# Optimization experiments

Hardware: AMD Instinct MI355X
Metric: run time of the kernel (lower is better)

Reference implementation:

```python
import jax, jax.numpy as jnp
import numpy as np

N = 1024   # nnodes
H = 8      # attention heads
C = 32     # gnn_repr_size (per head)
HC = H * C # 256
E = 65536  # num edges
ER = 32    # edge_repr_size
F = 3      # feat_emb_size
NUM_STOPS = 512


def setup_inputs() -> dict:
    key = jax.random.key(0)
    ks = jax.random.split(key, 24)
    g = lambda i, shape, s: jax.random.normal(ks[i], shape, dtype=jnp.float32) * s
    return {
        "dist": jax.random.uniform(ks[0], (N, N), dtype=jnp.float32),
        "stops": jax.random.randint(ks[1], (NUM_STOPS,), 0, N),
        "weekday": 3,
        "vehicles": 5,
        "markov": jax.random.uniform(ks[2], (N, N), dtype=jnp.float32),
        "demand": jax.random.uniform(ks[3], (N, 1), dtype=jnp.float32),
        "capacity": 10,
        "edge_index": jax.random.randint(ks[4], (2, E), 0, N),
        # GATConv layer 1 (in=1, out=H*C, edge_dim=1)
        "W1": g(5, (1, HC), 1.0), "We1": g(6, (1, HC), 1.0),
        "a_src1": g(7, (H, C), 0.1), "a_dst1": g(8, (H, C), 0.1), "a_edge1": g(9, (H, C), 0.1),
        "b1": jnp.zeros((HC,), jnp.float32),
        # GATConv layer 2 (in=H*C, out=H*C)
        "W2": g(10, (HC, HC), 0.0625), "We2": g(11, (1, HC), 1.0),
        "a_src2": g(12, (H, C), 0.1), "a_dst2": g(13, (H, C), 0.1), "a_edge2": g(14, (H, C), 0.1),
        "b2": jnp.zeros((HC,), jnp.float32),
        # edge summarizer Linear(2*HC, ER)
        "Wes": g(15, (2 * HC, ER), 0.0442), "bes": jnp.zeros((ER,), jnp.float32),
        # scalar embeddings
        "emb_weekday": g(16, (7, F), 0.1), "emb_capacity": g(17, (26, F), 0.1), "emb_vehicle": g(18, (15, F), 0.1),
        # combiner MLP: Linear(N*ER + 3N + 3F, N), Linear(N, N)
        "Wc1": g(19, (N * ER + 3 * N + 3 * F, N), 0.0053), "bc1": jnp.zeros((N,), jnp.float32),
        "Wc2": g(20, (N, N), 0.03125), "bc2": jnp.zeros((N,), jnp.float32),
    }


def _gat(x, src, dst, edge_attr, W, We, a_src, a_dst, a_edge, b):
    """PyG GATConv (concat heads, eval mode so attention dropout is identity)."""
    h = (x @ W).reshape(-1, H, C)                   # [N, H, C]
    e = (edge_attr @ We).reshape(-1, H, C)          # [E, H, C]
    alpha = (h * a_src).sum(-1)[src] + (h * a_dst).sum(-1)[dst] + (e * a_edge).sum(-1)  # [E, H]
    alpha = jax.nn.leaky_relu(alpha, 0.2)
    # segment softmax over destination nodes
    m = jax.ops.segment_max(alpha, dst, num_segments=N)
    m = jnp.where(jnp.isfinite(m), m, 0.0)
    ex = jnp.exp(alpha - m[dst])
    denom = jax.ops.segment_sum(ex, dst, num_segments=N)
    coef = ex / (denom[dst] + 1e-16)                # [E, H]
    out = jax.ops.segment_sum(h[src] * coef[:, :, None], dst, num_segments=N)  # [N, H, C]
    return out.reshape(-1, HC) + b


def reference(dist, stops, weekday, vehicles, markov, demand, capacity, edge_index,
              W1, We1, a_src1, a_dst1, a_edge1, b1,
              W2, We2, a_src2, a_dst2, a_edge2, b2,
              Wes, bes, emb_weekday, emb_capacity, emb_vehicle,
              Wc1, bc1, Wc2, bc2):
    src, dst = edge_index[0], edge_index[1]
    dist = (dist - dist.min()) / (dist.max() - dist.min())
    edge_attr = markov[src, dst][:, None]           # [E, 1]
    x = _gat(demand, src, dst, edge_attr, W1, We1, a_src1, a_dst1, a_edge1, b1)
    x = jax.nn.relu(x)
    x = _gat(x, src, dst, edge_attr, W2, We2, a_src2, a_dst2, a_edge2, b2)
    x = jax.nn.relu(x)                              # [N, HC]
    # edge_summarizer(cat(x_i, x_j)) decomposed: x_i @ Wes_top + x_j @ Wes_bot + bes
    ea = x @ Wes[:HC]                               # [N, ER]
    eb = x @ Wes[HC:]                               # [N, ER]
    edge_repr = (ea[:, None, :] + eb[None, :, :] + bes).reshape(N, N * ER)
    wf = jnp.broadcast_to(emb_weekday[weekday][None, :], (N, F))
    cf = jnp.broadcast_to(emb_capacity[capacity][None, :], (N, F))
    vf = jnp.broadcast_to(emb_vehicle[vehicles][None, :], (N, F))
    sf = jnp.zeros((N,), jnp.float32).at[stops].set(1.0)
    sf = jnp.broadcast_to(sf[None, :], (N, N))
    combined = jnp.concatenate([edge_repr, dist, markov, wf, cf, vf, sf], axis=1)
    out = jax.nn.relu(combined @ Wc1 + bc1) @ Wc2 + bc2  # [N, N]
    return out
```

## Files before the change

kernel.cpp:

```cpp
#include <hip/hip_runtime.h>

#define NN 1024
#define NE 65536

typedef short v8s __attribute__((ext_vector_type(8)));
typedef float v4f __attribute__((ext_vector_type(4)));

constexpr size_t OF_SCAL = 0;
constexpr size_t OF_MMP  = 64;
constexpr size_t OF_DEG  = 1088;
constexpr size_t OF_OFF  = 2112;
constexpr size_t OF_CUR  = 3200;
constexpr size_t OF_EIDX = 4224;
constexpr size_t OF_MARK = 69760;
constexpr size_t OF_T1   = 135296;
constexpr size_t OF_X1   = 143488;
constexpr size_t OF_H2   = 405632;
constexpr size_t OF_S2S  = 667776;
constexpr size_t OF_S2D  = 675968;
constexpr size_t OF_MAX2 = 684160;
constexpr size_t OF_DEN2 = 692352;
constexpr size_t OF_EX2  = 700544;
constexpr size_t OF_X2   = 1224832;
constexpr size_t OF_BCAT = 1486976;
constexpr size_t OF_EAB  = 1503360;
constexpr size_t OF_WVEC = 1568896;
constexpr size_t OF_SRP  = 1604800;
constexpr size_t OF_C0P  = 3701952;
constexpr size_t OF_SR   = 3775680;
constexpr size_t OF_BASE = 3808448;
constexpr size_t OF_AH   = 3809472;
constexpr size_t OF_AL   = 4874432;
constexpr size_t OF_BTH  = 5939392;
constexpr size_t OF_BTL  = 7004352;
constexpr size_t OF_HH   = 8069312;
constexpr size_t OF_HL   = 8593600;
constexpr size_t OF_W2TH = 9117888;
constexpr size_t OF_W2TL = 9642176;
constexpr size_t OF_P0   = 10166464;
constexpr size_t OF_P1   = 11215040;

__device__ inline unsigned short f2bf(float x){
  unsigned u = __float_as_uint(x);
  unsigned r = u + 0x7fffu + ((u>>16)&1u);
  return (unsigned short)(r>>16);
}
__device__ inline float bf2f(unsigned short h){
  return __uint_as_float(((unsigned)h)<<16);
}

__global__ void k_zero(int* deg){
  int i = blockIdx.x*256 + threadIdx.x;
  if (i < NN) deg[i] = 0;
}

__global__ void k_mm1(const float* __restrict__ dist, float* mnP, float* mxP){
  __shared__ float smn[256], smx[256];
  int tid = threadIdx.x;
  float mn = 1e30f, mx = -1e30f;
  for (int i = blockIdx.x*256 + tid; i < NN*NN; i += gridDim.x*256){
    float v = dist[i]; mn = fminf(mn, v); mx = fmaxf(mx, v);
  }
  smn[tid]=mn; smx[tid]=mx; __syncthreads();
  for (int s=128; s>0; s>>=1){
    if (tid<s){ smn[tid]=fminf(smn[tid],smn[tid+s]); smx[tid]=fmaxf(smx[tid],smx[tid+s]); }
    __syncthreads();
  }
  if (tid==0){ mnP[blockIdx.x]=smn[0]; mxP[blockIdx.x]=smx[0]; }
}

__global__ void k_mm2(const float* mnP, const float* mxP, float* scal){
  __shared__ float smn[512], smx[512];
  int tid = threadIdx.x;
  smn[tid]=mnP[tid]; smx[tid]=mxP[tid]; __syncthreads();
  for (int s=256; s>0; s>>=1){
    if (tid<s){ smn[tid]=fminf(smn[tid],smn[tid+s]); smx[tid]=fmaxf(smx[tid],smx[tid+s]); }
    __syncthreads();
  }
  if (tid==0){ scal[0]=smn[0]; scal[1]=1.0f/(smx[0]-smn[0]); }
}

__global__ void k_prep(const float* W1, const float* We1, const float* as1, const float* ad1,
                       const float* ae1, const float* We2, const float* ae2, float* scal){
  int t = threadIdx.x;
  if (t < 8){
    float s=0.f, d=0.f, e=0.f, e2=0.f;
    for (int c=0;c<32;c++){
      int i = t*32+c;
      s += W1[i]*as1[i]; d += W1[i]*ad1[i]; e += We1[i]*ae1[i]; e2 += We2[i]*ae2[i];
    }
    scal[16+t]=s; scal[24+t]=d; scal[32+t]=e; scal[40+t]=e2;
  }
}

__global__ void k_edges(const int* __restrict__ ei, const float* __restrict__ markov,
                        float* __restrict__ mark, int* __restrict__ deg){
  int e = blockIdx.x*256 + threadIdx.x;
  if (e >= NE) return;
  int s = ei[e], d = ei[NE+e];
  mark[e] = markov[(size_t)s*NN + d];
  atomicAdd(&deg[d], 1);
}

__global__ void k_scan(const int* deg, int* off, int* cur){
  __shared__ int tmp[NN];
  int t = threadIdx.x;
  tmp[t] = deg[t]; __syncthreads();
  for (int s=1; s<NN; s<<=1){
    int v = (t>=s) ? tmp[t-s] : 0;
    __syncthreads();
    tmp[t] += v;
    __syncthreads();
  }
  int ex = (t==0) ? 0 : tmp[t-1];
  off[t]=ex; cur[t]=ex;
  if (t==NN-1) off[NN]=tmp[NN-1];
}

__global__ void k_fill(const int* __restrict__ ei, int* __restrict__ cur, int* __restrict__ eidxl){
  int e = blockIdx.x*256 + threadIdx.x;
  if (e >= NE) return;
  int d = ei[NE+e];
  int p = atomicAdd(&cur[d], 1);
  eidxl[p] = e;
}

__global__ __launch_bounds__(64) void k_gat1(const int* __restrict__ ei, const int* __restrict__ eidxl,
    const int* __restrict__ off, const float* __restrict__ mark, const float* __restrict__ demand,
    const float* __restrict__ scal, float* __restrict__ t1){
  int n = blockIdx.x, lane = threadIdx.x;
  int o0 = off[n], o1 = off[n+1];
  float dn = demand[n];
  float cs[8], cd[8], ce[8], mx[8];
  #pragma unroll
  for (int h=0;h<8;h++){ cs[h]=scal[16+h]; cd[h]=scal[24+h]; ce[h]=scal[32+h]; mx[h]=-1e30f; }
  for (int i=o0+lane; i<o1; i+=64){
    int e = eidxl[i]; float ds = demand[ei[e]]; float me = mark[e];
    #pragma unroll
    for (int h=0;h<8;h++){
      float a = ds*cs[h] + dn*cd[h] + me*ce[h];
      a = a < 0.f ? 0.2f*a : a;
      mx[h] = fmaxf(mx[h], a);
    }
  }
  #pragma unroll
  for (int s=32; s>0; s>>=1){
    #pragma unroll
    for (int h=0;h<8;h++) mx[h] = fmaxf(mx[h], __shfl_xor(mx[h], s));
  }
  float se[8], sd_[8];
  #pragma unroll
  for (int h=0;h<8;h++){ se[h]=0.f; sd_[h]=0.f; }
  for (int i=o0+lane; i<o1; i+=64){
    int e = eidxl[i]; float ds = demand[ei[e]]; float me = mark[e];
    #pragma unroll
    for (int h=0;h<8;h++){
      float a = ds*cs[h] + dn*cd[h] + me*ce[h];
      a = a < 0.f ? 0.2f*a : a;
      float ex = expf(a - mx[h]);
      se[h] += ex; sd_[h] += ex*ds;
    }
  }
  #pragma unroll
  for (int s=32; s>0; s>>=1){
    #pragma unroll
    for (int h=0;h<8;h++){ se[h] += __shfl_xor(se[h], s); sd_[h] += __shfl_xor(sd_[h], s); }
  }
  if (lane==0){
    #pragma unroll
    for (int h=0;h<8;h++) t1[n*8+h] = sd_[h] / (se[h] + 1e-16f);
  }
}

__global__ void k_x1(const float* __restrict__ t1, const float* __restrict__ W1,
                     const float* __restrict__ b1, float* __restrict__ x1){
  int n = blockIdx.x, hc = threadIdx.x, h = hc >> 5;
  x1[(size_t)n*256 + hc] = fmaxf(t1[n*8+h]*W1[hc] + b1[hc], 0.f);
}

__global__ __launch_bounds__(256) void gemm64(const float* __restrict__ A, int lda,
    const float* __restrict__ B, int ldb, float* __restrict__ C, int ldc, int K,
    const float* __restrict__ bias, int dorelu){
  __shared__ float As[16][68];
  __shared__ float Bs[16][68];
  int tid = threadIdx.x;
  int tx = tid & 15, ty = tid >> 4;
  int row0 = ty*4, col0 = tx*4;
  int gm = blockIdx.y*64, gn = blockIdx.x*64;
  float acc[4][4] = {};
  for (int k0 = 0; k0 < K; k0 += 16){
    #pragma unroll
    for (int q=0;q<4;q++){
      int idx = tid*4+q; int i = idx>>4, kk = idx&15;
      As[kk][i] = A[(size_t)(gm+i)*lda + k0 + kk];
    }
    #pragma unroll
    for (int q=0;q<4;q++){
      int idx = tid*4+q; int kk = idx>>6, j = idx&63;
      Bs[kk][j] = B[(size_t)(k0+kk)*ldb + gn + j];
    }
    __syncthreads();
    #pragma unroll
    for (int kk=0;kk<16;kk++){
      float a0=As[kk][row0+0], a1=As[kk][row0+1], a2=As[kk][row0+2], a3=As[kk][row0+3];
      float b0=Bs[kk][col0+0], b1=Bs[kk][col0+1], b2=Bs[kk][col0+2], b3=Bs[kk][col0+3];
      acc[0][0]+=a0*b0; acc[0][1]+=a0*b1; acc[0][2]+=a0*b2; acc[0][3]+=a0*b3;
      acc[1][0]+=a1*b0; acc[1][1]+=a1*b1; acc[1][2]+=a1*b2; acc[1][3]+=a1*b3;
      acc[2][0]+=a2*b0; acc[2][1]+=a2*b1; acc[2][2]+=a2*b2; acc[2][3]+=a2*b3;
      acc[3][0]+=a3*b0; acc[3][1]+=a3*b1; acc[3][2]+=a3*b2; acc[3][3]+=a3*b3;
    }
    __syncthreads();
  }
  #pragma unroll
  for (int i=0;i<4;i++){
    #pragma unroll
    for (int j=0;j<4;j++){
      int cc = gn + col0 + j;
      float v = acc[i][j];
      if (bias) v += bias[cc];
      if (dorelu) v = fmaxf(v, 0.f);
      C[(size_t)(gm+row0+i)*ldc + cc] = v;
    }
  }
}

__global__ void k_s2(const float* __restrict__ h2, const float* __restrict__ as2,
                     const float* __restrict__ ad2, float* __restrict__ s2s, float* __restrict__ s2d){
  int idx = blockIdx.x*256 + threadIdx.x;
  if (idx >= NN*8) return;
  int n = idx >> 3, h = idx & 7;
  float ss = 0.f, sd = 0.f;
  for (int c=0;c<32;c++){
    float v = h2[(size_t)n*256 + h*32 + c];
    ss += v*as2[h*32+c]; sd += v*ad2[h*32+c];
  }
  s2s[idx]=ss; s2d[idx]=sd;
}

__global__ __launch_bounds__(64) void k_gat2max(const int* __restrict__ ei, const int* __restrict__ eidxl,
    const int* __restrict__ off, const float* __restrict__ mark, const float* __restrict__ s2s,
    const float* __restrict__ s2d, const float* __restrict__ scal,
    float* __restrict__ mx2, float* __restrict__ den){
  int n = blockIdx.x, lane = threadIdx.x;
  int o0 = off[n], o1 = off[n+1];
  float ce[8], sdn[8], mx[8];
  #pragma unroll
  for (int h=0;h<8;h++){ ce[h]=scal[40+h]; sdn[h]=s2d[n*8+h]; mx[h]=-1e30f; }
  for (int i=o0+lane; i<o1; i+=64){
    int e = eidxl[i]; int s = ei[e]; float me = mark[e];
    #pragma unroll
    for (int h=0;h<8;h++){
      float a = s2s[s*8+h] + sdn[h] + me*ce[h];
      a = a < 0.f ? 0.2f*a : a;
      mx[h] = fmaxf(mx[h], a);
    }
  }
  #pragma unroll
  for (int sft=32; sft>0; sft>>=1){
    #pragma unroll
    for (int h=0;h<8;h++) mx[h] = fmaxf(mx[h], __shfl_xor(mx[h], sft));
  }
  float se[8];
  #pragma unroll
  for (int h=0;h<8;h++) se[h]=0.f;
  for (int i=o0+lane; i<o1; i+=64){
    int e = eidxl[i]; int s = ei[e]; float me = mark[e];
    #pragma unroll
    for (int h=0;h<8;h++){
      float a = s2s[s*8+h] + sdn[h] + me*ce[h];
      a = a < 0.f ? 0.2f*a : a;
      se[h] += expf(a - mx[h]);
    }
  }
  #pragma unroll
  for (int sft=32; sft>0; sft>>=1){
    #pragma unroll
    for (int h=0;h<8;h++) se[h] += __shfl_xor(se[h], sft);
  }
  if (lane==0){
    #pragma unroll
    for (int h=0;h<8;h++){ mx2[n*8+h] = (o1>o0) ? mx[h] : 0.f; den[n*8+h] = se[h]; }
  }
}

__global__ void k_ex2(const int* __restrict__ ei, const float* __restrict__ mark,
                      const float* __restrict__ s2s, const float* __restrict__ s2d,
                      const float* __restrict__ mx2, const float* __restrict__ scal,
                      float* __restrict__ ex2){
  int e = blockIdx.x*256 + threadIdx.x;
  if (e >= NE) return;
  int s = ei[e], d = ei[NE+e];
  float me = mark[e];
  #pragma unroll
  for (int h=0;h<8;h++){
    float a = s2s[s*8+h] + s2d[d*8+h] + me*scal[40+h];
    a = a < 0.f ? 0.2f*a : a;
    ex2[(size_t)e*8+h] = expf(a - mx2[d*8+h]);
  }
}

__global__ __launch_bounds__(256) void k_agg2(const int* __restrict__ ei, const int* __restrict__ eidxl,
    const int* __restrict__ off, const float* __restrict__ ex2, const float* __restrict__ den,
    const float* __restrict__ h2, const float* __restrict__ b2, float* __restrict__ x2){
  __shared__ int eL[64], sL[64];
  int n = blockIdx.x, tid = threadIdx.x, h = tid >> 5;
  int o0 = off[n], o1 = off[n+1];
  float inv = 1.0f/(den[n*8+h] + 1e-16f);
  float acc = 0.f;
  for (int b = o0; b < o1; b += 64){
    int len = min(64, o1 - b);
    __syncthreads();
    if (tid < len){ int e = eidxl[b+tid]; eL[tid]=e; sL[tid]=ei[e]; }
    __syncthreads();
    for (int j=0;j<len;j++){
      acc += ex2[(size_t)eL[j]*8 + h] * h2[(size_t)sL[j]*256 + tid];
    }
  }
  x2[(size_t)n*256 + tid] = fmaxf(acc*inv + b2[tid], 0.f);
}

__global__ void k_bcat(const float* __restrict__ Wes, float* __restrict__ Bcat){
  int idx = blockIdx.x*256 + threadIdx.x;
  if (idx >= 256*64) return;
  int k = idx >> 6, r = idx & 63;
  Bcat[idx] = (r < 32) ? Wes[(size_t)k*32 + r] : Wes[(size_t)(256+k)*32 + (r-32)];
}

__global__ void k_wvec(const float* __restrict__ eab, const float* __restrict__ bes,
                       const float* __restrict__ ew, const float* __restrict__ ec, const float* __restrict__ ev,
                       const int* __restrict__ wd, const int* __restrict__ cap, const int* __restrict__ veh,
                       float* __restrict__ wvec){
  int m = blockIdx.x*256 + threadIdx.x;
  if (m >= 35849) return;
  float v;
  if (m < 32768){ int j = m >> 5, r = m & 31; v = eab[(size_t)j*64 + 32 + r] + bes[r]; }
  else if (m < 34816) v = 0.f;
  else if (m < 34819) v = ew[wd[0]*3 + (m-34816)];
  else if (m < 34822) v = ec[cap[0]*3 + (m-34819)];
  else if (m < 34825) v = ev[veh[0]*3 + (m-34822)];
  else v = 0.f;
  wvec[m] = v;
}

__global__ void k_stops(const int* __restrict__ stops, float* __restrict__ wvec){
  wvec[34825 + stops[threadIdx.x]] = 1.0f;
}

__global__ __launch_bounds__(256) void k_src0(const float* __restrict__ Wc1, const float* __restrict__ wvec,
                                              float* __restrict__ srP, float* __restrict__ c0P){
  __shared__ float c0s[256*4];
  int t = threadIdx.x;
  int kg = t & 31;
  int rg = t >> 5;
  int col = blockIdx.x*128 + kg*4;
  int chunk = blockIdx.y;
  int m0 = chunk*512;
  float sr[4][4];
  #pragma unroll
  for (int u=0;u<4;u++){ sr[u][0]=0.f; sr[u][1]=0.f; sr[u][2]=0.f; sr[u][3]=0.f; }
  float c0a[4] = {0.f,0.f,0.f,0.f};
  for (int jj=0; jj<16; ++jj){
    int rbase = m0 + jj*32 + rg*4;
    #pragma unroll
    for (int u=0;u<4;u++){
      int m = rbase + u;
      float4 w = make_float4(0.f,0.f,0.f,0.f);
      float wv = 0.f;
      if (m < 35849){
        w = *reinterpret_cast<const float4*>(&Wc1[(size_t)m*1024 + col]);
        wv = wvec[m];
      }
      c0a[0] += wv*w.x; c0a[1] += wv*w.y; c0a[2] += wv*w.z; c0a[3] += wv*w.w;
      if (chunk < 64){
        sr[u][0] += w.x; sr[u][1] += w.y; sr[u][2] += w.z; sr[u][3] += w.w;
      }
    }
  }
  if (chunk < 64){
    #pragma unroll
    for (int u=0;u<4;u++){
      int r = rg*4 + u;
      float4 v = make_float4(sr[u][0], sr[u][1], sr[u][2], sr[u][3]);
      *reinterpret_cast<float4*>(&srP[(size_t)(chunk*32 + r)*1024 + col]) = v;
    }
  }
  c0s[t*4+0]=c0a[0]; c0s[t*4+1]=c0a[1]; c0s[t*4+2]=c0a[2]; c0s[t*4+3]=c0a[3];
  __syncthreads();
  if (t < 32){
    float s0=0.f,s1=0.f,s2=0.f,s3=0.f;
    #pragma unroll
    for (int q=0;q<8;q++){
      int b = (t + q*32)*4;
      s0 += c0s[b+0]; s1 += c0s[b+1]; s2 += c0s[b+2]; s3 += c0s[b+3];
    }
    float4 v = make_float4(s0,s1,s2,s3);
    *reinterpret_cast<float4*>(&c0P[(size_t)chunk*1024 + blockIdx.x*128 + t*4]) = v;
  }
}

__global__ void k_stage2(const float* __restrict__ srP, const float* __restrict__ c0P,
                         const float* __restrict__ bc1, float* __restrict__ Sr, float* __restrict__ base){
  int idx = blockIdx.x*256 + threadIdx.x;
  if (idx < 8192){
    int r = idx >> 8, k4 = idx & 255;
    float s0=0.f,s1=0.f,s2=0.f,s3=0.f;
    for (int c=0;c<64;c++){
      float4 v = *reinterpret_cast<const float4*>(&srP[(size_t)(c*32 + r)*1024 + k4*4]);
      s0+=v.x; s1+=v.y; s2+=v.z; s3+=v.w;
    }
    float4 o = make_float4(s0,s1,s2,s3);
    *reinterpret_cast<float4*>(&Sr[(size_t)r*1024 + k4*4]) = o;
  } else if (idx < 8448){
    int k4 = idx - 8192;
    float4 b = *reinterpret_cast<const float4*>(&bc1[k4*4]);
    float s0=b.x, s1=b.y, s2=b.z, s3=b.w;
    for (int c=0;c<71;c++){
      float4 v = *reinterpret_cast<const float4*>(&c0P[(size_t)c*1024 + k4*4]);
      s0+=v.x; s1+=v.y; s2+=v.z; s3+=v.w;
    }
    float4 o = make_float4(s0,s1,s2,s3);
    *reinterpret_cast<float4*>(&base[k4*4]) = o;
  }
}

__global__ void k_cvtA(const float* __restrict__ dist, const float* __restrict__ markov,
                       const float* __restrict__ eab, const float* __restrict__ scal,
                       unsigned short* __restrict__ Ah, unsigned short* __restrict__ Al){
  int k = blockIdx.x*256 + threadIdx.x;
  int i = blockIdx.y;
  if (k >= 2080) return;
  float mn = scal[0], inv = scal[1];
  float v;
  if (k < 1024) v = (dist[(size_t)i*1024 + k] - mn)*inv;
  else if (k < 2048) v = markov[(size_t)i*1024 + (k-1024)];
  else v = eab[(size_t)i*64 + (k-2048)];
  unsigned short h = f2bf(v);
  Ah[(size_t)i*2080 + k] = h;
  Al[(size_t)i*2080 + k] = f2bf(v - bf2f(h));
}

__global__ void k_cvtT(const float* __restrict__ src, const float* __restrict__ src2, int k2,
                       int ldt, unsigned short* __restrict__ Th, unsigned short* __restrict__ Tl){
  __shared__ unsigned short shh[32][65], shl[32][65];
  int t = threadIdx.x;
  int k0 = blockIdx.x*32, n0 = blockIdx.y*64;
  #pragma unroll
  for (int q=0;q<8;q++){
    int idx = t + q*256;
    int kl = idx >> 6, nl = idx & 63;
    int k = k0 + kl;
    float v = (k < k2) ? src[(size_t)k*1024 + n0 + nl] : src2[(size_t)(k-k2)*1024 + n0 + nl];
    unsigned short h = f2bf(v);
    shh[kl][nl] = h;
    shl[kl][nl] = f2bf(v - bf2f(h));
  }
  __syncthreads();
  #pragma unroll
  for (int q=0;q<8;q++){
    int idx = t + q*256;
    int nl = idx >> 5, kl = idx & 31;
    Th[(size_t)(n0+nl)*ldt + k0 + kl] = shh[kl][nl];
    Tl[(size_t)(n0+nl)*ldt + k0 + kl] = shl[kl][nl];
  }
}

__global__ __launch_bounds__(256) void k_mfma64(
    const unsigned short* __restrict__ Ah, const unsigned short* __restrict__ Al, int lda,
    const unsigned short* __restrict__ Bth, const unsigned short* __restrict__ Btl, int ldb,
    float* __restrict__ Cp, int kSteps, int kTot){
  __shared__ __align__(16) unsigned short Ash[64*32], Asl[64*32], Bsh[64*32], Bsl[64*32];
  int t = threadIdx.x;
  int wave = t >> 6, lane = t & 63;
  int wr = wave >> 1, wc = wave & 1;
  int gm = blockIdx.y*64, gn = blockIdx.x*64;
  Cp += (size_t)blockIdx.z << 20;
  int ks0 = blockIdx.z * kSteps;
  int ks1 = ks0 + kSteps; if (ks1 > kTot) ks1 = kTot;

  int sr = t >> 2, ss = t & 3;
  int kq = lane >> 4;
  int l15 = lane & 15;
  int rA0 = wr*32 + l15;
  int cB0 = wc*32 + l15;

  v4f acc[2][2];
  #pragma unroll
  for (int i=0;i<2;i++)
    #pragma unroll
    for (int j=0;j<2;j++) acc[i][j] = (v4f){0.f,0.f,0.f,0.f};

  for (int ks = ks0; ks < ks1; ++ks){
    int kb = ks*32;
    v8s ga_h = *(const v8s*)(Ah  + (size_t)(gm+sr)*lda + kb + ss*8);
    v8s ga_l = *(const v8s*)(Al  + (size_t)(gm+sr)*lda + kb + ss*8);
    v8s gb_h = *(const v8s*)(Bth + (size_t)(gn+sr)*ldb + kb + ss*8);
    v8s gb_l = *(const v8s*)(Btl + (size_t)(gn+sr)*ldb + kb + ss*8);
    __syncthreads();
    int woff = sr*32 + ((ss ^ (sr&3))*8);
    *(v8s*)(Ash + woff) = ga_h;
    *(v8s*)(Asl + woff) = ga_l;
    *(v8s*)(Bsh + woff) = gb_h;
    *(v8s*)(Bsl + woff) = gb_l;
    __syncthreads();
    #pragma unroll
    for (int fi=0; fi<2; fi++){
      int ra = rA0 + fi*16;
      int aoff = ra*32 + ((kq ^ (ra&3))*8);
      v8s fa_h = *(v8s*)(Ash + aoff);
      v8s fa_l = *(v8s*)(Asl + aoff);
      #pragma unroll
      for (int fj=0; fj<2; fj++){
        int cb = cB0 + fj*16;
        int boff = cb*32 + ((kq ^ (cb&3))*8);
        v8s fb_h = *(v8s*)(Bsh + boff);
        v8s fb_l = *(v8s*)(Bsl + boff);
        acc[fi][fj] = __builtin_amdgcn_mfma_f32_16x16x32_bf16(fa_h, fb_h, acc[fi][fj], 0, 0, 0);
        acc[fi][fj] = __builtin_amdgcn_mfma_f32_16x16x32_bf16(fa_h, fb_l, acc[fi][fj], 0, 0, 0);
        acc[fi][fj] = __builtin_amdgcn_mfma_f32_16x16x32_bf16(fa_l, fb_h, acc[fi][fj], 0, 0, 0);
      }
    }
  }
  int row0 = gm + wr*32 + (lane>>4)*4;
  int col0 = gn + wc*32 + l15;
  #pragma unroll
  for (int fi=0; fi<2; fi++)
    #pragma unroll
    for (int fj=0; fj<2; fj++)
      #pragma unroll
      for (int r=0; r<4; r++)
        Cp[(size_t)(row0 + fi*16 + r)*1024 + col0 + fj*16] = acc[fi][fj][r];
}

__global__ void k_fin_hidden(const float* __restrict__ P0, const float* __restrict__ P1,
                             const float* __restrict__ base,
                             unsigned short* __restrict__ Hh, unsigned short* __restrict__ Hl){
  int idx = blockIdx.x*256 + threadIdx.x;
  float v = P0[idx] + P1[idx] + base[idx & 1023];
  v = fmaxf(v, 0.f);
  unsigned short h = f2bf(v);
  Hh[idx] = h;
  Hl[idx] = f2bf(v - bf2f(h));
}

__global__ void k_fin_out(const float* __restrict__ P0, const float* __restrict__ P1,
                          const float* __restrict__ bc2, float* __restrict__ out){
  int idx = blockIdx.x*256 + threadIdx.x;
  out[idx] = P0[idx] + P1[idx] + bc2[idx & 1023];
}

extern "C" void kernel_launch(void* const* d_in, const int* in_sizes, int n_in,
                              void* d_out, int out_size, void* d_ws, size_t ws_size,
                              hipStream_t stream){
  const float* dist     = (const float*)d_in[0];
  const int*   stops    = (const int*)  d_in[1];
  const int*   weekday  = (const int*)  d_in[2];
  const int*   vehicles = (const int*)  d_in[3];
  const float* markov   = (const float*)d_in[4];
  const float* demand   = (const float*)d_in[5];
  const int*   capacity = (const int*)  d_in[6];
  const int*   ei       = (const int*)  d_in[7];
  const float* W1  = (const float*)d_in[8];
  const float* We1 = (const float*)d_in[9];
  const float* as1 = (const float*)d_in[10];
  const float* ad1 = (const float*)d_in[11];
  const float* ae1 = (const float*)d_in[12];
  const float* b1  = (const float*)d_in[13];
  const float* W2  = (const float*)d_in[14];
  const float* We2 = (const float*)d_in[15];
  const float* as2 = (const float*)d_in[16];
  const float* ad2 = (const float*)d_in[17];
  const float* ae2 = (const float*)d_in[18];
  const float* b2  = (const float*)d_in[19];
  const float* Wes = (const float*)d_in[20];
  const float* bes = (const float*)d_in[21];
  const float* ew  = (const float*)d_in[22];
  const float* ec  = (const float*)d_in[23];
  const float* ev  = (const float*)d_in[24];
  const float* Wc1 = (const float*)d_in[25];
  const float* bc1 = (const float*)d_in[26];
  const float* Wc2 = (const float*)d_in[27];
  const float* bc2 = (const float*)d_in[28];

  float* W    = (float*)d_ws;
  float* scal = W + OF_SCAL;
  float* mmP  = W + OF_MMP;
  int*   deg  = (int*)(W + OF_DEG);
  int*   off  = (int*)(W + OF_OFF);
  int*   cur  = (int*)(W + OF_CUR);
  int*   eidxl= (int*)(W + OF_EIDX);
  float* mark = W + OF_MARK;
  float* t1   = W + OF_T1;
  float* x1   = W + OF_X1;
  float* h2   = W + OF_H2;
  float* s2s  = W + OF_S2S;
  float* s2d  = W + OF_S2D;
  float* mx2  = W + OF_MAX2;
  float* den2 = W + OF_DEN2;
  float* ex2  = W + OF_EX2;
  float* x2   = W + OF_X2;
  float* Bcat = W + OF_BCAT;
  float* eab  = W + OF_EAB;
  float* wvec = W + OF_WVEC;
  float* srP  = W + OF_SRP;
  float* c0P  = W + OF_C0P;
  float* Sr   = W + OF_SR;
  float* base = W + OF_BASE;
  unsigned short* Ah   = (unsigned short*)(W + OF_AH);
  unsigned short* Al   = (unsigned short*)(W + OF_AL);
  unsigned short* Bth  = (unsigned short*)(W + OF_BTH);
  unsigned short* Btl  = (unsigned short*)(W + OF_BTL);
  unsigned short* Hh   = (unsigned short*)(W + OF_HH);
  unsigned short* Hl   = (unsigned short*)(W + OF_HL);
  unsigned short* W2th = (unsigned short*)(W + OF_W2TH);
  unsigned short* W2tl = (unsigned short*)(W + OF_W2TL);
  float* P0   = W + OF_P0;
  float* out  = (float*)d_out;

  k_zero<<<dim3(4), dim3(256), 0, stream>>>(deg);
  k_mm1 <<<dim3(512), dim3(256), 0, stream>>>(dist, mmP, mmP+512);
  k_mm2 <<<dim3(1), dim3(512), 0, stream>>>(mmP, mmP+512, scal);
  k_prep<<<dim3(1), dim3(64), 0, stream>>>(W1, We1, as1, ad1, ae1, We2, ae2, scal);
  k_edges<<<dim3(256), dim3(256), 0, stream>>>(ei, markov, mark, deg);
  k_scan<<<dim3(1), dim3(1024), 0, stream>>>(deg, off, cur);
  k_fill<<<dim3(256), dim3(256), 0, stream>>>(ei, cur, eidxl);
  k_gat1<<<dim3(1024), dim3(64), 0, stream>>>(ei, eidxl, off, mark, demand, scal, t1);
  k_x1  <<<dim3(1024), dim3(256), 0, stream>>>(t1, W1, b1, x1);
  gemm64<<<dim3(4,16), dim3(256), 0, stream>>>(x1, 256, W2, 256, h2, 256, 256, (const float*)nullptr, 0);
  k_s2  <<<dim3(32), dim3(256), 0, stream>>>(h2, as2, ad2, s2s, s2d);
  k_gat2max<<<dim3(1024), dim3(64), 0, stream>>>(ei, eidxl, off, mark, s2s, s2d, scal, mx2, den2);
  k_ex2 <<<dim3(256), dim3(256), 0, stream>>>(ei, mark, s2s, s2d, mx2, scal, ex2);
  k_agg2<<<dim3(1024), dim3(256), 0, stream>>>(ei, eidxl, off, ex2, den2, h2, b2, x2);
  k_bcat<<<dim3(64), dim3(256), 0, stream>>>(Wes, Bcat);
  gemm64<<<dim3(1,16), dim3(256), 0, stream>>>(x2, 256, Bcat, 64, eab, 64, 256, (const float*)nullptr, 0);
  k_wvec<<<dim3(141), dim3(256), 0, stream>>>(eab, bes, ew, ec, ev, weekday, capacity, vehicles, wvec);
  k_stops<<<dim3(1), dim3(512), 0, stream>>>(stops, wvec);
  k_src0<<<dim3(8,71), dim3(256), 0, stream>>>(Wc1, wvec, srP, c0P);
  k_stage2<<<dim3(33), dim3(256), 0, stream>>>(srP, c0P, bc1, Sr, base);
  k_cvtA<<<dim3(9,1024), dim3(256), 0, stream>>>(dist, markov, eab, scal, Ah, Al);
  k_cvtT<<<dim3(65,16), dim3(256), 0, stream>>>(Wc1 + (size_t)32768*1024, Sr, 2048, 2080, Bth, Btl);
  k_cvtT<<<dim3(32,16), dim3(256), 0, stream>>>(Wc2, Wc2, 1<<30, 1024, W2th, W2tl);
  k_mfma64<<<dim3(16,16,2), dim3(256), 0, stream>>>(Ah, Al, 2080, Bth, Btl, 2080, P0, 33, 65);
  k_fin_hidden<<<dim3(4096), dim3(256), 0, stream>>>(P0, P0 + (1<<20), base, Hh, Hl);
  k_mfma64<<<dim3(16,16,2), dim3(256), 0, stream>>>(Hh, Hl, 1024, W2th, W2tl, 1024, P0, 16, 32);
  k_fin_out<<<dim3(4096), dim3(256), 0, stream>>>(P0, P0 + (1<<20), bc2, out);
}
```

Measured before the change: 221.3 us.

## Enlarge split-K MFMA GEMM tiles to 128x128 and split K four ways

The split-bf16 MFMA GEMM moves from 64x64 to 128x128 output tiles, with each wave computing a 4x4 grid of 16x16 fragments. B fragments are hoisted out of the row loop, and the LDS swizzle changes to suit the new layout. This aims to raise data reuse per LDS load and cut global traffic per FLOP. To keep the grid at 256 blocks, split-K grows from 2 to 4 partial planes, which adds partial-sum writes and reads. The reduction/finalize kernels are vectorized to float4 and sum four planes, which needs a larger workspace region for the partials.

```diff
diff --git a/kernel.cpp b/kernel.cpp
--- a/kernel.cpp
+++ b/kernel.cpp
@@ -38,7 +38,6 @@
 constexpr size_t OF_W2TH = 9117888;
 constexpr size_t OF_W2TL = 9642176;
 constexpr size_t OF_P0   = 10166464;
-constexpr size_t OF_P1   = 11215040;
 
 __device__ inline unsigned short f2bf(float x){
   unsigned u = __float_as_uint(x);
@@ -464,88 +463,114 @@
   }
 }
 
-__global__ __launch_bounds__(256) void k_mfma64(
+__global__ __launch_bounds__(256) void k_mfma128(
     const unsigned short* __restrict__ Ah, const unsigned short* __restrict__ Al, int lda,
     const unsigned short* __restrict__ Bth, const unsigned short* __restrict__ Btl, int ldb,
     float* __restrict__ Cp, int kSteps, int kTot){
-  __shared__ __align__(16) unsigned short Ash[64*32], Asl[64*32], Bsh[64*32], Bsl[64*32];
+  __shared__ __align__(16) unsigned short Ash[128*32], Asl[128*32], Bsh[128*32], Bsl[128*32];
   int t = threadIdx.x;
   int wave = t >> 6, lane = t & 63;
   int wr = wave >> 1, wc = wave & 1;
-  int gm = blockIdx.y*64, gn = blockIdx.x*64;
-  Cp += (size_t)blockIdx.z << 20;
+  int gm = blockIdx.y*128, gn = blockIdx.x*128;
+  float* plane = Cp + ((size_t)blockIdx.z << 20);
   int ks0 = blockIdx.z * kSteps;
   int ks1 = ks0 + kSteps; if (ks1 > kTot) ks1 = kTot;
 
-  int sr = t >> 2, ss = t & 3;
   int kq = lane >> 4;
   int l15 = lane & 15;
-  int rA0 = wr*32 + l15;
-  int cB0 = wc*32 + l15;
-
-  v4f acc[2][2];
-  #pragma unroll
-  for (int i=0;i<2;i++)
-    #pragma unroll
-    for (int j=0;j<2;j++) acc[i][j] = (v4f){0.f,0.f,0.f,0.f};
+
+  int r0s = t >> 2,        s0s = t & 3;
+  int r1s = (t+256) >> 2,  s1s = t & 3;
+
+  v4f acc[4][4];
+  #pragma unroll
+  for (int i=0;i<4;i++)
+    #pragma unroll
+    for (int j=0;j<4;j++) acc[i][j] = (v4f){0.f,0.f,0.f,0.f};
 
   for (int ks = ks0; ks < ks1; ++ks){
     int kb = ks*32;
-    v8s ga_h = *(const v8s*)(Ah  + (size_t)(gm+sr)*lda + kb + ss*8);
-    v8s ga_l = *(const v8s*)(Al  + (size_t)(gm+sr)*lda + kb + ss*8);
-    v8s gb_h = *(const v8s*)(Bth + (size_t)(gn+sr)*ldb + kb + ss*8);
-    v8s gb_l = *(const v8s*)(Btl + (size_t)(gn+sr)*ldb + kb + ss*8);
-    __syncthreads();
-    int woff = sr*32 + ((ss ^ (sr&3))*8);
-    *(v8s*)(Ash + woff) = ga_h;
-    *(v8s*)(Asl + woff) = ga_l;
-    *(v8s*)(Bsh + woff) = gb_h;
-    *(v8s*)(Bsl + woff) = gb_l;
-    __syncthreads();
-    #pragma unroll
-    for (int fi=0; fi<2; fi++){
-      int ra = rA0 + fi*16;
-      int aoff = ra*32 + ((kq ^ (ra&3))*8);
-      v8s fa_h = *(v8s*)(Ash + aoff);
-      v8s fa_l = *(v8s*)(Asl + aoff);
+    const size_t a0 = (size_t)(gm+r0s)*lda + kb + s0s*8;
+    const size_t a1 = (size_t)(gm+r1s)*lda + kb + s1s*8;
+    const size_t b0 = (size_t)(gn+r0s)*ldb + kb + s0s*8;
+    const size_t b1 = (size_t)(gn+r1s)*ldb + kb + s1s*8;
+    v8s gah0 = *(const v8s*)(Ah + a0), gah1 = *(const v8s*)(Ah + a1);
+    v8s gal0 = *(const v8s*)(Al + a0), gal1 = *(const v8s*)(Al + a1);
+    v8s gbh0 = *(const v8s*)(Bth + b0), gbh1 = *(const v8s*)(Bth + b1);
+    v8s gbl0 = *(const v8s*)(Btl + b0), gbl1 = *(const v8s*)(Btl + b1);
+    __syncthreads();
+    int w0 = r0s*32 + ((s0s ^ ((r0s>>1)&3))*8);
+    int w1 = r1s*32 + ((s1s ^ ((r1s>>1)&3))*8);
+    *(v8s*)(Ash + w0) = gah0;  *(v8s*)(Ash + w1) = gah1;
+    *(v8s*)(Asl + w0) = gal0;  *(v8s*)(Asl + w1) = gal1;
+    *(v8s*)(Bsh + w0) = gbh0;  *(v8s*)(Bsh + w1) = gbh1;
+    *(v8s*)(Bsl + w0) = gbl0;  *(v8s*)(Bsl + w1) = gbl1;
+    __syncthreads();
+    v8s fbh[4], fbl[4];
+    #pragma unroll
+    for (int fj=0; fj<4; fj++){
+      int cb = wc*64 + fj*16 + l15;
+      int boff = cb*32 + ((kq ^ ((cb>>1)&3))*8);
+      fbh[fj] = *(v8s*)(Bsh + boff);
+      fbl[fj] = *(v8s*)(Bsl + boff);
+    }
+    #pragma unroll
+    for (int fi=0; fi<4; fi++){
+      int ra = wr*64 + fi*16 + l15;
+      int aoff = ra*32 + ((kq ^ ((ra>>1)&3))*8);
+      v8s fah = *(v8s*)(Ash + aoff);
+      v8s fal = *(v8s*)(Asl + aoff);
       #pragma unroll
-      for (int fj=0; fj<2; fj++){
-        int cb = cB0 + fj*16;
-        int boff = cb*32 + ((kq ^ (cb&3))*8);
-        v8s fb_h = *(v8s*)(Bsh + boff);
-        v8s fb_l = *(v8s*)(Bsl + boff);
-        acc[fi][fj] = __builtin_amdgcn_mfma_f32_16x16x32_bf16(fa_h, fb_h, acc[fi][fj], 0, 0, 0);
-        acc[fi][fj] = __builtin_amdgcn_mfma_f32_16x16x32_bf16(fa_h, fb_l, acc[fi][fj], 0, 0, 0);
-        acc[fi][fj] = __builtin_amdgcn_mfma_f32_16x16x32_bf16(fa_l, fb_h, acc[fi][fj], 0, 0, 0);
+      for (int fj=0; fj<4; fj++){
+        acc[fi][fj] = __builtin_amdgcn_mfma_f32_16x16x32_bf16(fah, fbh[fj], acc[fi][fj], 0, 0, 0);
+        acc[fi][fj] = __builtin_amdgcn_mfma_f32_16x16x32_bf16(fah, fbl[fj], acc[fi][fj], 0, 0, 0);
+        acc[fi][fj] = __builtin_amdgcn_mfma_f32_16x16x32_bf16(fal, fbh[fj], acc[fi][fj], 0, 0, 0);
       }
     }
   }
-  int row0 = gm + wr*32 + (lane>>4)*4;
-  int col0 = gn + wc*32 + l15;
-  #pragma unroll
-  for (int fi=0; fi<2; fi++)
-    #pragma unroll
-    for (int fj=0; fj<2; fj++)
+  int row0 = gm + wr*64 + (lane>>4)*4;
+  int col0 = gn + wc*64 + l15;
+  #pragma unroll
+  for (int fi=0; fi<4; fi++)
+    #pragma unroll
+    for (int fj=0; fj<4; fj++)
       #pragma unroll
       for (int r=0; r<4; r++)
-        Cp[(size_t)(row0 + fi*16 + r)*1024 + col0 + fj*16] = acc[fi][fj][r];
-}
-
-__global__ void k_fin_hidden(const float* __restrict__ P0, const float* __restrict__ P1,
-                             const float* __restrict__ base,
+        plane[(size_t)(row0 + fi*16 + r)*1024 + col0 + fj*16] = acc[fi][fj][r];
+}
+
+__global__ void k_fin_hidden(const float* __restrict__ P, const float* __restrict__ base,
                              unsigned short* __restrict__ Hh, unsigned short* __restrict__ Hl){
   int idx = blockIdx.x*256 + threadIdx.x;
-  float v = P0[idx] + P1[idx] + base[idx & 1023];
-  v = fmaxf(v, 0.f);
-  unsigned short h = f2bf(v);
-  Hh[idx] = h;
-  Hl[idx] = f2bf(v - bf2f(h));
-}
-
-__global__ void k_fin_out(const float* __restrict__ P0, const float* __restrict__ P1,
-                          const float* __restrict__ bc2, float* __restrict__ out){
+  float4 v0 = *reinterpret_cast<const float4*>(P + (size_t)idx*4);
+  float4 v1 = *reinterpret_cast<const float4*>(P + (1u<<20) + (size_t)idx*4);
+  float4 v2 = *reinterpret_cast<const float4*>(P + (2u<<20) + (size_t)idx*4);
+  float4 v3 = *reinterpret_cast<const float4*>(P + (3u<<20) + (size_t)idx*4);
+  float4 b  = *reinterpret_cast<const float4*>(base + ((idx & 255)*4));
+  float v[4] = { v0.x+v1.x+v2.x+v3.x+b.x, v0.y+v1.y+v2.y+v3.y+b.y,
+                 v0.z+v1.z+v2.z+v3.z+b.z, v0.w+v1.w+v2.w+v3.w+b.w };
+  unsigned short hh[4], hl[4];
+  #pragma unroll
+  for (int q=0;q<4;q++){
+    float x = fmaxf(v[q], 0.f);
+    hh[q] = f2bf(x);
+    hl[q] = f2bf(x - bf2f(hh[q]));
+  }
+  *reinterpret_cast<uint2*>(Hh + (size_t)idx*4) = *reinterpret_cast<uint2*>(hh);
+  *reinterpret_cast<uint2*>(Hl + (size_t)idx*4) = *reinterpret_cast<uint2*>(hl);
+}
+
+__global__ void k_fin_out(const float* __restrict__ P, const float* __restrict__ bc2,
+                          float* __restrict__ out){
   int idx = blockIdx.x*256 + threadIdx.x;
-  out[idx] = P0[idx] + P1[idx] + bc2[idx & 1023];
+  float4 v0 = *reinterpret_cast<const float4*>(P + (size_t)idx*4);
+  float4 v1 = *reinterpret_cast<const float4*>(P + (1u<<20) + (size_t)idx*4);
+  float4 v2 = *reinterpret_cast<const float4*>(P + (2u<<20) + (size_t)idx*4);
+  float4 v3 = *reinterpret_cast<const float4*>(P + (3u<<20) + (size_t)idx*4);
+  float4 b  = *reinterpret_cast<const float4*>(bc2 + ((idx & 255)*4));
+  float4 o = make_float4(v0.x+v1.x+v2.x+v3.x+b.x, v0.y+v1.y+v2.y+v3.y+b.y,
+                         v0.z+v1.z+v2.z+v3.z+b.z, v0.w+v1.w+v2.w+v3.w+b.w);
+  *reinterpret_cast<float4*>(out + (size_t)idx*4) = o;
 }
 
 extern "C" void kernel_launch(void* const* d_in, const int* in_sizes, int n_in,
@@ -639,8 +664,8 @@
   k_cvtA<<<dim3(9,1024), dim3(256), 0, stream>>>(dist, markov, eab, scal, Ah, Al);
   k_cvtT<<<dim3(65,16), dim3(256), 0, stream>>>(Wc1 + (size_t)32768*1024, Sr, 2048, 2080, Bth, Btl);
   k_cvtT<<<dim3(32,16), dim3(256), 0, stream>>>(Wc2, Wc2, 1<<30, 1024, W2th, W2tl);
-  k_mfma64<<<dim3(16,16,2), dim3(256), 0, stream>>>(Ah, Al, 2080, Bth, Btl, 2080, P0, 33, 65);
-  k_fin_hidden<<<dim3(4096), dim3(256), 0, stream>>>(P0, P0 + (1<<20), base, Hh, Hl);
-  k_mfma64<<<dim3(16,16,2), dim3(256), 0, stream>>>(Hh, Hl, 1024, W2th, W2tl, 1024, P0, 16, 32);
-  k_fin_out<<<dim3(4096), dim3(256), 0, stream>>>(P0, P0 + (1<<20), bc2, out);
-}
+  k_mfma128<<<dim3(8,8,4), dim3(256), 0, stream>>>(Ah, Al, 2080, Bth, Btl, 2080, P0, 17, 65);
+  k_fin_hidden<<<dim3(1024), dim3(256), 0, stream>>>(P0, base, Hh, Hl);
+  k_mfma128<<<dim3(8,8,4), dim3(256), 0, stream>>>(Hh, Hl, 1024, W2th, W2tl, 1024, P0, 8, 32);
+  k_fin_out<<<dim3(1024), dim3(256), 0, stream>>>(P0, bc2, out);
+}
```

Measured after the change: 224.8 us. No clear change (+1.6%).
